# Kernel tuning notes

Hardware: AMD Instinct MI355X
Metric: run time of the kernel (lower is better)

## Reference

```python
import jax, jax.numpy as jnp
import numpy as np

BN_EPS = 1e-5

def _bn(x, p):
    # p: [4, C] = (gamma, beta, running_mean, running_var); inference-mode BN
    g, b, m, v = p[0], p[1], p[2], p[3]
    if x.ndim == 3:  # [B, C, N]
        g, b, m, v = g[:, None], b[:, None], m[:, None], v[:, None]
    return g * (x - m) * jax.lax.rsqrt(v + BN_EPS) + b

def _angle_density(xyz, npoints=32):
    # xyz: [B, N, 3]; pairwise cosine distance via a single GEMM instead of expand
    inner = jnp.einsum('bnc,bmc->bnm', xyz, xyz)            # [B, N, N]
    nrm = jnp.sqrt(jnp.sum(xyz * xyz, axis=-1))             # [B, N]
    dist = 1.0 - inner / (nrm[:, :, None] * nrm[:, None, :])
    neg_vals, _ = jax.lax.top_k(-dist, npoints)             # k smallest distances
    feat_density = jnp.mean(-neg_vals, axis=-1)             # [B, N]
    inv = 1.0 / feat_density
    return inv / jnp.max(inv)                               # global max, as in torch

def _density_attn(x, density, wqk, wt, bt, bnp):
    # x: [B, C, N]; density: [B, 1, N]; wqk: [C//4, 1] (q_conv and k_conv share weights)
    xk = wqk * density                                      # [B, C//4, N] (1x1 conv, 1 in-ch)
    energy = jnp.einsum('bdn,bdm->bnm', xk, xk)             # x_q == x_k.T (shared weight)
    attn = jax.nn.softmax(energy, axis=-1)
    attn = attn / (1e-9 + jnp.sum(attn, axis=1, keepdims=True))
    x_r = jnp.einsum('bcn,bnm->bcm', x, attn)               # [B, C, N]
    y = jnp.einsum('oc,bcn->bon', wt, x - x_r) + bt[:, None]
    return x + jax.nn.relu(_bn(y, bnp))

def _conv_bn_relu(x, w, bnp):
    return jax.nn.relu(_bn(jnp.einsum('oc,bcn->bon', w, x), bnp))

def _forward(x, w1, w2, w3, w4, w5, bn1, bn2, bn3, bn4, bn5,
             da1_wqk, da1_wt, da1_bt, da1_bn,
             da2_wqk, da2_wt, da2_bt, da2_bn,
             da3_wqk, da3_wt, da3_bt, da3_bn,
             da4_wqk, da4_wt, da4_bt, da4_bn,
             lin1_w, bn6, lin2_w, lin2_b):
    dens = _angle_density(jnp.transpose(x, (0, 2, 1)), 32)[:, None, :]  # [B, 1, N]
    h = _conv_bn_relu(x, w1, bn1)
    h = _density_attn(h, dens, da1_wqk, da1_wt, da1_bt, da1_bn)
    h = _conv_bn_relu(h, w2, bn2)
    h = _density_attn(h, dens, da2_wqk, da2_wt, da2_bt, da2_bn)
    h = _conv_bn_relu(h, w3, bn3)
    h = _density_attn(h, dens, da3_wqk, da3_wt, da3_bt, da3_bn)
    h = _conv_bn_relu(h, w4, bn4)
    h = _density_attn(h, dens, da4_wqk, da4_wt, da4_bt, da4_bn)
    h = _conv_bn_relu(h, w5, bn5)                           # [B, 1024, N]
    h = jnp.max(h, axis=-1)                                 # adaptive_max_pool1d -> [B, 1024]
    h = jax.nn.relu(_bn(h @ lin1_w.T, bn6))                 # [B, 512]; dropout is identity in eval
    return h @ lin2_w.T + lin2_b                            # [B, num_classes]

def setup_inputs() -> dict:
    key = jax.random.key(0)
    ki = iter(jax.random.split(key, 80))
    def rn(shape, s):
        return jax.random.normal(next(ki), shape, jnp.float32) * s
    def bnp(c):
        return jnp.stack([
            jax.random.uniform(next(ki), (c,), jnp.float32, 0.5, 1.5),  # gamma
            rn((c,), 0.05),                                             # beta
            rn((c,), 0.1),                                              # running_mean
            jax.random.uniform(next(ki), (c,), jnp.float32, 0.5, 1.5),  # running_var
        ])
    B, N, E = 16, 2048, 1024
    d = {}
    d['x'] = jax.random.normal(next(ki), (B, 3, N), jnp.float32)
    d['w1'] = rn((64, 3), 0.5)
    d['w2'] = rn((64, 64), 0.125)
    d['w3'] = rn((64, 64), 0.125)
    d['w4'] = rn((128, 64), 0.125)
    d['w5'] = rn((E, 128), 0.09)
    d['bn1'], d['bn2'], d['bn3'] = bnp(64), bnp(64), bnp(64)
    d['bn4'], d['bn5'] = bnp(128), bnp(E)
    for i, c in zip((1, 2, 3, 4), (64, 64, 64, 128)):
        d[f'da{i}_wqk'] = rn((c // 4, 1), 1.0)
        d[f'da{i}_wt'] = rn((c, c), 1.0 / np.sqrt(c))
        d[f'da{i}_bt'] = rn((c,), 0.05)
        d[f'da{i}_bn'] = bnp(c)
    d['lin1_w'] = rn((512, E), 1.0 / np.sqrt(E))
    d['bn6'] = bnp(512)
    d['lin2_w'] = rn((40, 512), 1.0 / np.sqrt(512))
    d['lin2_b'] = rn((40,), 0.05)
    return d

def reference(x, w1, w2, w3, w4, w5, bn1, bn2, bn3, bn4, bn5,
              da1_wqk, da1_wt, da1_bt, da1_bn,
              da2_wqk, da2_wt, da2_bt, da2_bn,
              da3_wqk, da3_wt, da3_bt, da3_bn,
              da4_wqk, da4_wt, da4_bt, da4_bn,
              lin1_w, bn6, lin2_w, lin2_b):
    return _forward(x, w1, w2, w3, w4, w5, bn1, bn2, bn3, bn4, bn5,
                    da1_wqk, da1_wt, da1_bt, da1_bn,
                    da2_wqk, da2_wt, da2_bt, da2_bn,
                    da3_wqk, da3_wt, da3_bt, da3_bn,
                    da4_wqk, da4_wt, da4_bt, da4_bn,
                    lin1_w, bn6, lin2_w, lin2_b)
```

## Files before the change

kernel.cpp:

```cpp
#include <hip/hip_runtime.h>
#include <math.h>

#define BB 16
#define NN 2048
#define BN_EPS_ 1e-5f

typedef __attribute__((ext_vector_type(8))) short short8v;
typedef __attribute__((ext_vector_type(4))) float f32x4;

__device__ __forceinline__ unsigned short f2bf(float x){
  unsigned u = __float_as_uint(x);
  u += 0x7fffu + ((u >> 16) & 1u);
  return (unsigned short)(u >> 16);
}
__device__ __forceinline__ float bf2f(unsigned short h){
  return __uint_as_float(((unsigned)h) << 16);
}

__global__ __launch_bounds__(256) void normalize_points_kernel(const float* __restrict__ x,
        float* __restrict__ u){
  int idx = blockIdx.x*256 + threadIdx.x;
  int b = idx >> 11, n = idx & (NN-1);
  const float* xb = x + (size_t)b*3*NN;
  float x0 = xb[n], x1 = xb[NN+n], x2 = xb[2*NN+n];
  float rn = rsqrtf(x0*x0 + x1*x1 + x2*x2);
  float* ub = u + (size_t)b*3*NN;
  ub[n] = x0*rn; ub[NN+n] = x1*rn; ub[2*NN+n] = x2*rn;
}

#define DG 8
__global__ __launch_bounds__(256) void density5_kernel(const float* __restrict__ u,
        float* __restrict__ inv, float* __restrict__ blockmax){
  __shared__ float us0[NN], us1[NN], us2[NN];
  __shared__ unsigned int hist[DG][256];
  __shared__ float buf[DG][128];
  __shared__ unsigned int bufcnt[DG];
  __shared__ unsigned int bB[DG], bC0[DG];
  __shared__ float partial[DG][4];
  __shared__ float rowiv[DG];
  const int b = blockIdx.y;
  const float* ub = u + (size_t)b*3*NN;
  const int t = threadIdx.x;
  #pragma unroll
  for (int i = 0; i < NN/(256*4); ++i){
    int n4 = t + 256*i;
    ((float4*)us0)[n4] = ((const float4*)ub)[n4];
    ((float4*)us1)[n4] = ((const float4*)(ub+NN))[n4];
    ((float4*)us2)[n4] = ((const float4*)(ub+2*NN))[n4];
  }
  #pragma unroll
  for (int i = 0; i < DG; ++i) hist[i][t & 255] = 0u;
  if (t < DG) bufcnt[t] = 0u;
  __syncthreads();
  float m0[8], m1[8], m2[8];
  #pragma unroll
  for (int i = 0; i < 8; ++i){
    int c = t + 256*i;
    m0[i] = us0[c]; m1[i] = us1[c]; m2[i] = us2[c];
  }
  const int r0 = blockIdx.x * DG;
  float ru0[DG], ru1[DG], ru2[DG];
  #pragma unroll
  for (int j = 0; j < DG; ++j){ ru0[j] = us0[r0+j]; ru1[j] = us1[r0+j]; ru2[j] = us2[r0+j]; }

  unsigned qp[DG][2];
  #pragma unroll
  for (int j = 0; j < DG; ++j){
    unsigned q0 = 0u, q1 = 0u;
    #pragma unroll
    for (int i = 0; i < 8; ++i){
      float d = 1.0f - (ru0[j]*m0[i] + ru1[j]*m1[i] + ru2[j]*m2[i]);
      int q = (int)(d * 128.0f);
      q = q < 0 ? 0 : (q > 255 ? 255 : q);
      if (i < 4) q0 |= (unsigned)q << (8*i); else q1 |= (unsigned)q << (8*(i-4));
      atomicAdd(&hist[j][q], 1u);
    }
    qp[j][0] = q0; qp[j][1] = q1;
  }
  __syncthreads();

  const int wave = t >> 6, lane = t & 63;
  #pragma unroll
  for (int jj = 0; jj < 2; ++jj){
    const int j = 2*wave + jj;
    uint4 cc = *(const uint4*)&hist[j][lane*4];
    unsigned tl = cc.x + cc.y + cc.z + cc.w;
    unsigned inc = tl;
    #pragma unroll
    for (int off = 1; off < 64; off <<= 1){
      unsigned o = __shfl_up(inc, off);
      if (lane >= off) inc += o;
    }
    unsigned base = inc - tl;
    if (base < 32u && base + tl >= 32u){
      unsigned cum = base;
      if (cum < 32u && cum + cc.x >= 32u){ bB[j] = lane*4 + 0; bC0[j] = cum; } cum += cc.x;
      if (cum < 32u && cum + cc.y >= 32u){ bB[j] = lane*4 + 1; bC0[j] = cum; } cum += cc.y;
      if (cum < 32u && cum + cc.z >= 32u){ bB[j] = lane*4 + 2; bC0[j] = cum; } cum += cc.z;
      if (cum < 32u && cum + cc.w >= 32u){ bB[j] = lane*4 + 3; bC0[j] = cum; } cum += cc.w;
    }
  }
  __syncthreads();

  #pragma unroll
  for (int j = 0; j < DG; ++j){
    const int B = (int)bB[j];
    float s = 0.0f;
    #pragma unroll
    for (int i = 0; i < 8; ++i){
      float d = 1.0f - (ru0[j]*m0[i] + ru1[j]*m1[i] + ru2[j]*m2[i]);
      const int q = (int)((qp[j][i>>2] >> (8*(i&3))) & 255u);
      if (q < B) s += d;
      else if (q == B){
        unsigned slot = atomicAdd(&bufcnt[j], 1u);
        if (slot < 128u) buf[j][slot] = d;
      }
    }
    #pragma unroll
    for (int off = 32; off > 0; off >>= 1) s += __shfl_xor(s, off);
    if (lane == 0) partial[j][wave] = s;
  }
  __syncthreads();

  #pragma unroll
  for (int jj = 0; jj < 2; ++jj){
    const int j = 2*wave + jj;
    float total = partial[j][0] + partial[j][1] + partial[j][2] + partial[j][3];
    int cnt = (int)bufcnt[j]; if (cnt > 128) cnt = 128;
    const int rr = 32 - (int)bC0[j];
    float v1 = (lane      < cnt) ? buf[j][lane]      : 0.0f;
    float v2 = (lane + 64 < cnt) ? buf[j][lane + 64] : 0.0f;
    int rk1 = 0, rk2 = 0;
    for (int k = 0; k < cnt; ++k){
      float vk = buf[j][k];
      rk1 += ((vk < v1) || (vk == v1 && k < lane)) ? 1 : 0;
      rk2 += ((vk < v2) || (vk == v2 && k < lane + 64)) ? 1 : 0;
    }
    float contrib = ((lane      < cnt) && (rk1 < rr)) ? v1 : 0.0f;
    contrib      += ((lane + 64 < cnt) && (rk2 < rr)) ? v2 : 0.0f;
    #pragma unroll
    for (int off = 32; off > 0; off >>= 1) contrib += __shfl_xor(contrib, off);
    total += contrib;
    if (lane == 0){
      float iv = 32.0f / total;
      inv[b*NN + r0 + j] = iv;
      rowiv[j] = iv;
    }
  }
  __syncthreads();
  if (t == 0){
    float m = rowiv[0];
    #pragma unroll
    for (int j = 1; j < DG; ++j) m = fmaxf(m, rowiv[j]);
    blockmax[blockIdx.y * gridDim.x + blockIdx.x] = m;
  }
}

__global__ __launch_bounds__(256) void finalize_max_kernel(const float* __restrict__ blockmax,
        float* __restrict__ maxout){
  __shared__ float pw[4];
  const int t = threadIdx.x;
  float m = 0.0f;
  #pragma unroll
  for (int i = 0; i < 16; ++i) m = fmaxf(m, blockmax[t + 256*i]);
  #pragma unroll
  for (int off = 32; off > 0; off >>= 1) m = fmaxf(m, __shfl_xor(m, off));
  if ((t & 63) == 0) pw[t >> 6] = m;
  __syncthreads();
  if (t == 0) *maxout = fmaxf(fmaxf(pw[0], pw[1]), fmaxf(pw[2], pw[3]));
}

__global__ void normalize_kernel(float* __restrict__ dens, const float* __restrict__ maxval){
  int i = blockIdx.x*256 + threadIdx.x;
  float mx = *maxval;
  dens[i] = dens[i] / mx;
}

__global__ __launch_bounds__(256) void zrow_kernel(const float* __restrict__ dens,
      const float* __restrict__ wqk, int K, float* __restrict__ out){
  __shared__ float ds[NN];
  const int b = blockIdx.y, t = threadIdx.x;
  float s = 0.0f;
  for (int k = 0; k < K; ++k){ float w = wqk[k]; s += w*w; }
  #pragma unroll
  for (int i = 0; i < NN/256; ++i) ds[t + 256*i] = dens[b*NN + t + 256*i];
  __syncthreads();
  const int wave = t >> 6, lane = t & 63;
  const int RPB = NN / gridDim.x;
  const int r0 = blockIdx.x * RPB;
  for (int r = r0 + wave; r < r0 + RPB; r += 4){
    float a = s * ds[r];
    float sum = 0.0f;
    #pragma unroll
    for (int i = 0; i < NN/64; ++i){
      int m = lane + 64*i;
      sum += __expf(a * ds[m]);
    }
    #pragma unroll
    for (int off = 32; off > 0; off >>= 1) sum += __shfl_xor(sum, off);
    if (lane == 0) out[b*NN + r] = 1.0f/sum;
  }
}

template<int C>
__global__ __launch_bounds__(256, 2) void attn_mfma_kernel(const unsigned short* __restrict__ Ah,
      const unsigned short* __restrict__ Al, const float* __restrict__ dens,
      const float* __restrict__ zinv, const float* __restrict__ wqk, int K,
      float* __restrict__ raw){
  constexpr int RA = C + 16;
  constexpr int RH = C / 32;
  __shared__ __align__(16) unsigned short ah[C][64], al[C][64];
  __shared__ __align__(16) unsigned short eh[64][64], el[64][64];
  const int id = blockIdx.x;
  const int b  = (id & 7) + ((id >> 8) << 3);
  const int m0 = ((id >> 3) & 31) * 64;
  const int t = threadIdx.x;
  float s = 0.0f;
  for (int k = 0; k < K; ++k){ float w = wqk[k]; s += w*w; }
  const float* db = dens + b*NN;
  const float* zb = zinv + b*NN;
  const unsigned short* Abh = Ah + (size_t)b*C*NN;
  const unsigned short* Abl = Al + (size_t)b*C*NN;
  const int ej = t >> 2, ekq = (t & 3) * 16;
  const float dmj = db[m0 + ej];
  const unsigned swe = (unsigned)((ej & 7) << 4);
  const int l = t & 63, w = t >> 6;
  const int rw = w & 1, cw = w >> 1;
  const int fc = l & 15, g = l >> 4;
  const unsigned swr = (unsigned)((fc & 7) << 4);
  short8v ones8, zero8;
  #pragma unroll
  for (int q = 0; q < 8; ++q){ ones8[q] = (short)0x3F80; zero8[q] = 0; }
  f32x4 acc[RH][2], cs[2];
  #pragma unroll
  for (int i = 0; i < RH; ++i){ acc[i][0] = (f32x4){0.f,0.f,0.f,0.f}; acc[i][1] = (f32x4){0.f,0.f,0.f,0.f}; }
  cs[0] = (f32x4){0.f,0.f,0.f,0.f}; cs[1] = (f32x4){0.f,0.f,0.f,0.f};

  for (int n0 = 0; n0 < NN; n0 += 64){
    __syncthreads();
    #pragma unroll
    for (int i = 0; i < C*8/256; ++i){
      int idx = t + 256*i;
      int row = idx >> 3, c8 = (idx & 7) * 8;
      unsigned off = (unsigned)(row*128) + (((unsigned)(c8*2)) ^ ((unsigned)((row&7)<<4)));
      *(uint4*)((char*)ah + off) = *(const uint4*)(Abh + (size_t)row*NN + n0 + c8);
      *(uint4*)((char*)al + off) = *(const uint4*)(Abl + (size_t)row*NN + n0 + c8);
    }
    {
      unsigned hp[8], lp[8];
      #pragma unroll
      for (int u = 0; u < 4; ++u){
        float4 dn = *(const float4*)(db + n0 + ekq + u*4);
        float4 zv = *(const float4*)(zb + n0 + ekq + u*4);
        float e0 = zv.x*__expf(s*dn.x*dmj), e1 = zv.y*__expf(s*dn.y*dmj);
        float e2 = zv.z*__expf(s*dn.z*dmj), e3 = zv.w*__expf(s*dn.w*dmj);
        unsigned short a0=f2bf(e0), a1=f2bf(e1), a2=f2bf(e2), a3=f2bf(e3);
        hp[u*2+0] = (unsigned)a0 | ((unsigned)a1<<16);
        hp[u*2+1] = (unsigned)a2 | ((unsigned)a3<<16);
        lp[u*2+0] = (unsigned)f2bf(e0-bf2f(a0)) | ((unsigned)f2bf(e1-bf2f(a1))<<16);
        lp[u*2+1] = (unsigned)f2bf(e2-bf2f(a2)) | ((unsigned)f2bf(e3-bf2f(a3))<<16);
      }
      unsigned row = (unsigned)(ej*128);
      unsigned o1 = row + (((unsigned)(ekq*2))      ^ swe);
      unsigned o2 = row + (((unsigned)(ekq*2 + 16)) ^ swe);
      *(uint4*)((char*)eh + o1) = make_uint4(hp[0],hp[1],hp[2],hp[3]);
      *(uint4*)((char*)eh + o2) = make_uint4(hp[4],hp[5],hp[6],hp[7]);
      *(uint4*)((char*)el + o1) = make_uint4(lp[0],lp[1],lp[2],lp[3]);
      *(uint4*)((char*)el + o2) = make_uint4(lp[4],lp[5],lp[6],lp[7]);
    }
    __syncthreads();
    #pragma unroll
    for (int kk = 0; kk < 2; ++kk){
      unsigned ko = ((unsigned)((kk*32 + g*8)*2)) ^ swr;
      short8v bh[2], bl[2], ai[RH], au[RH];
      #pragma unroll
      for (int ct = 0; ct < 2; ++ct){
        unsigned eoff = (unsigned)(((2*cw + ct)*16 + fc)*128) + ko;
        bh[ct] = *(const short8v*)((const char*)eh + eoff);
        bl[ct] = *(const short8v*)((const char*)el + eoff);
      }
      #pragma unroll
      for (int i = 0; i < RH; ++i){
        unsigned aoff = (unsigned)((rw*(C/2) + i*16 + fc)*128) + ko;
        ai[i] = *(const short8v*)((const char*)ah + aoff);
        au[i] = *(const short8v*)((const char*)al + aoff);
      }
      #pragma unroll
      for (int i = 0; i < RH; ++i){
        #pragma unroll
        for (int ct = 0; ct < 2; ++ct){
          acc[i][ct] = __builtin_amdgcn_mfma_f32_16x16x32_bf16(ai[i], bh[ct], acc[i][ct], 0, 0, 0);
          acc[i][ct] = __builtin_amdgcn_mfma_f32_16x16x32_bf16(ai[i], bl[ct], acc[i][ct], 0, 0, 0);
          acc[i][ct] = __builtin_amdgcn_mfma_f32_16x16x32_bf16(au[i], bh[ct], acc[i][ct], 0, 0, 0);
        }
      }
      if (rw == 1){
        short8v ac = (fc == 0) ? ones8 : zero8;
        #pragma unroll
        for (int ct = 0; ct < 2; ++ct){
          cs[ct] = __builtin_amdgcn_mfma_f32_16x16x32_bf16(ac, bh[ct], cs[ct], 0, 0, 0);
          cs[ct] = __builtin_amdgcn_mfma_f32_16x16x32_bf16(ac, bl[ct], cs[ct], 0, 0, 0);
        }
      }
    }
  }
  #pragma unroll
  for (int ct = 0; ct < 2; ++ct){
    float* rb = raw + (size_t)b*RA*NN + m0 + (2*cw + ct)*16 + fc;
    #pragma unroll
    for (int i = 0; i < RH; ++i){
      #pragma unroll
      for (int r = 0; r < 4; ++r){
        int row = rw*(C/2) + i*16 + g*4 + r;
        rb[(size_t)row*NN] = acc[i][ct][r];
      }
    }
    if (rw == 1){
      #pragma unroll
      for (int r = 0; r < 4; ++r){
        int row = C + g*4 + r;
        rb[(size_t)row*NN] = cs[ct][r];
      }
    }
  }
}

template<int C, bool TP>
__global__ __launch_bounds__(256) void attn_post_kernel(const float* __restrict__ x,
      const float* __restrict__ raw, const float* __restrict__ wt,
      const float* __restrict__ bt, const float* __restrict__ bnp,
      float* __restrict__ out, unsigned short* __restrict__ th,
      unsigned short* __restrict__ tl){
  constexpr int RA = C + 16;
  __shared__ float ds[32][68];
  __shared__ float ws[32][C+4];
  __shared__ float cbs[64];
  const int b = blockIdx.y, m0 = blockIdx.x*64, t = threadIdx.x;
  const float* xb = x + (size_t)b*C*NN;
  const float* rb = raw + (size_t)b*RA*NN;
  if (t < 64) cbs[t] = 1.0f / (1e-9f + rb[(size_t)C*NN + m0 + t]);
  const int tr = t >> 4, tc = t & 15;
  constexpr int R = C/16;
  float acc[R][4];
  #pragma unroll
  for (int i = 0; i < R; ++i){ acc[i][0]=acc[i][1]=acc[i][2]=acc[i][3]=0.0f; }
  for (int c0 = 0; c0 < C; c0 += 32){
    __syncthreads();
    #pragma unroll
    for (int i = 0; i < 8; ++i){
      int idx = t + 256*i;
      int m = idx & 63, cl = idx >> 6;
      int cc = c0 + cl;
      ds[cl][m] = xb[cc*NN + m0 + m] - rb[cc*NN + m0 + m] * cbs[m];
    }
    #pragma unroll
    for (int i = 0; i < C*32/256; ++i){
      int idx = t + 256*i;
      int cl = idx & 31, o = idx >> 5;
      ws[cl][o] = wt[o*C + c0 + cl];
    }
    __syncthreads();
    #pragma unroll
    for (int k = 0; k < 32; ++k){
      float4 e = *(const float4*)&ds[k][tc*4];
      float a[R];
      #pragma unroll
      for (int q = 0; q < R/4; ++q)
        *(float4*)&a[q*4] = *(const float4*)&ws[k][tr*R + q*4];
      #pragma unroll
      for (int i = 0; i < R; ++i){
        acc[i][0] += a[i]*e.x; acc[i][1] += a[i]*e.y;
        acc[i][2] += a[i]*e.z; acc[i][3] += a[i]*e.w;
      }
    }
  }
  #pragma unroll
  for (int i = 0; i < R; ++i){
    int o = tr*R + i;
    float g = bnp[o], be = bnp[C+o], mn = bnp[2*C+o], vv = bnp[3*C+o];
    float sc = g * rsqrtf(vv + BN_EPS_);
    float sh = be - mn*sc;
    float bv = bt[o];
    #pragma unroll
    for (int j = 0; j < 4; ++j){
      float y = acc[i][j] + bv;
      y = sc*y + sh;
      y = fmaxf(y, 0.0f);
      acc[i][j] = xb[o*NN + m0 + tc*4 + j] + y;
    }
    if (!TP)
      *(float4*)&out[((size_t)b*C + o)*NN + m0 + tc*4] =
          make_float4(acc[i][0], acc[i][1], acc[i][2], acc[i][3]);
  }
  if (TP){
    unsigned short* Ts = (unsigned short*)&ws[0][0];
    #pragma unroll
    for (int pass = 0; pass < 2; ++pass){
      __syncthreads();
      #pragma unroll
      for (int q = 0; q < R/2; ++q){
        #pragma unroll
        for (int j = 0; j < 4; ++j){
          int n = tc*4 + j;
          float y0 = acc[2*q][j], y1 = acc[2*q+1][j];
          unsigned short a0 = f2bf(y0), a1 = f2bf(y1);
          unsigned short v0 = pass ? f2bf(y0 - bf2f(a0)) : a0;
          unsigned short v1 = pass ? f2bf(y1 - bf2f(a1)) : a1;
          unsigned off = (unsigned)(n*256) +
              (((unsigned)((tr*R + 2*q)*2)) ^ ((unsigned)((n&7)<<4)));
          *(unsigned*)((char*)Ts + off) = (unsigned)v0 | ((unsigned)v1<<16);
        }
      }
      __syncthreads();
      unsigned short* gout = (pass ? tl : th) + ((size_t)b*NN + m0)*128;
      int n = t >> 2;
      #pragma unroll
      for (int s2 = 0; s2 < 4; ++s2){
        int sl = (t&3)*4 + s2;
        unsigned off = (unsigned)(n*256) + ((unsigned)((sl ^ (n&7)) << 4));
        uint4 v = *(const uint4*)((const char*)Ts + off);
        *(uint4*)(gout + (size_t)n*128 + sl*8) = v;
      }
    }
  }
}

template<int CIN, int COUT>
__global__ __launch_bounds__(256) void conv_bn_relu_kernel(const float* __restrict__ x,
      const float* __restrict__ w, const float* __restrict__ bnp, float* __restrict__ out,
      unsigned short* __restrict__ oh, unsigned short* __restrict__ ol){
  constexpr int CH = (CIN < 32) ? CIN : 32;
  __shared__ float xs[CH][68];
  __shared__ float ws[CH][COUT+4];
  const int b = blockIdx.y, m0 = blockIdx.x*64, t = threadIdx.x;
  const float* xb = x + (size_t)b*CIN*NN;
  const int tr = t >> 4, tc = t & 15;
  constexpr int R = COUT/16;
  float acc[R][4];
  #pragma unroll
  for (int i = 0; i < R; ++i){ acc[i][0]=acc[i][1]=acc[i][2]=acc[i][3]=0.0f; }
  for (int c0 = 0; c0 < CIN; c0 += CH){
    __syncthreads();
    for (int idx = t; idx < CH*64; idx += 256){
      int m = idx & 63, cl = idx >> 6;
      xs[cl][m] = xb[(c0+cl)*NN + m0 + m];
    }
    for (int idx = t; idx < CH*COUT; idx += 256){
      int cl = idx % CH, o = idx / CH;
      ws[cl][o] = w[o*CIN + c0 + cl];
    }
    __syncthreads();
    #pragma unroll
    for (int k = 0; k < CH; ++k){
      float4 e = *(const float4*)&xs[k][tc*4];
      float a[R];
      #pragma unroll
      for (int q = 0; q < R/4; ++q)
        *(float4*)&a[q*4] = *(const float4*)&ws[k][tr*R + q*4];
      #pragma unroll
      for (int i = 0; i < R; ++i){
        acc[i][0] += a[i]*e.x; acc[i][1] += a[i]*e.y;
        acc[i][2] += a[i]*e.z; acc[i][3] += a[i]*e.w;
      }
    }
  }
  #pragma unroll
  for (int i = 0; i < R; ++i){
    int o = tr*R + i;
    float g = bnp[o], be = bnp[COUT+o], mn = bnp[2*COUT+o], vv = bnp[3*COUT+o];
    float sc = g * rsqrtf(vv + BN_EPS_);
    float sh = be - mn*sc;
    float4 r;
    float* rp = &r.x;
    #pragma unroll
    for (int j = 0; j < 4; ++j){
      float y = sc*acc[i][j] + sh;
      rp[j] = fmaxf(y, 0.0f);
    }
    size_t base = ((size_t)b*COUT + o)*NN + m0 + tc*4;
    *(float4*)&out[base] = r;
    unsigned short h0=f2bf(r.x), h1=f2bf(r.y), h2=f2bf(r.z), h3=f2bf(r.w);
    uint2 hp, lp;
    hp.x = (unsigned)h0 | ((unsigned)h1<<16);
    hp.y = (unsigned)h2 | ((unsigned)h3<<16);
    lp.x = (unsigned)f2bf(r.x-bf2f(h0)) | ((unsigned)f2bf(r.y-bf2f(h1))<<16);
    lp.y = (unsigned)f2bf(r.z-bf2f(h2)) | ((unsigned)f2bf(r.w-bf2f(h3))<<16);
    *(uint2*)&oh[base] = hp;
    *(uint2*)&ol[base] = lp;
  }
}

__global__ __launch_bounds__(256, 2) void conv5_mfma_kernel(
      const unsigned short* __restrict__ hTh, const unsigned short* __restrict__ hTl,
      const float* __restrict__ w5, const float* __restrict__ bnp,
      float* __restrict__ pooled){
  __shared__ __align__(16) unsigned short wh[64][128], wl[64][128];
  __shared__ __align__(16) unsigned short hh[64][128], hl[64][128];
  const int id = blockIdx.x;
  const int b  = (id & 7) + ((id >> 9) << 3);
  const int inner = (id >> 3) & 63;
  const int o0 = (inner & 15) * 64;
  const int nb = (inner >> 4) * (NN/4);
  const int t = threadIdx.x;
  const int l = t & 63, w = t >> 6;
  const int rw = w & 1, cw = w >> 1;
  const int fc = l & 15, g = l >> 4;
  const unsigned swr = (unsigned)((fc & 7) << 4);
  #pragma unroll
  for (int i = 0; i < 8; ++i){
    int idx = t + 256*i;
    int row = idx >> 5, c0 = (idx & 31) * 4;
    float4 v = *(const float4*)(w5 + (size_t)(o0 + row)*128 + c0);
    unsigned short h0=f2bf(v.x), h1=f2bf(v.y), h2=f2bf(v.z), h3=f2bf(v.w);
    uint2 hp, lp;
    hp.x = (unsigned)h0 | ((unsigned)h1<<16);
    hp.y = (unsigned)h2 | ((unsigned)h3<<16);
    lp.x = (unsigned)f2bf(v.x-bf2f(h0)) | ((unsigned)f2bf(v.y-bf2f(h1))<<16);
    lp.y = (unsigned)f2bf(v.z-bf2f(h2)) | ((unsigned)f2bf(v.w-bf2f(h3))<<16);
    unsigned off = (unsigned)(row*256) + (((unsigned)(c0*2)) ^ ((unsigned)((row&7)<<4)));
    *(uint2*)((char*)wh + off) = hp;
    *(uint2*)((char*)wl + off) = lp;
  }
  float sc[2][4], sh[2][4];
  #pragma unroll
  for (int i = 0; i < 2; ++i){
    #pragma unroll
    for (int r = 0; r < 4; ++r){
      int o = o0 + rw*32 + i*16 + g*4 + r;
      float gg = bnp[o], be = bnp[1024+o], mn = bnp[2048+o], vv = bnp[3072+o];
      sc[i][r] = gg * rsqrtf(vv + BN_EPS_);
      sh[i][r] = be - mn*sc[i][r];
    }
  }
  float vmax[2][4] = {{0.f,0.f,0.f,0.f},{0.f,0.f,0.f,0.f}};
  const unsigned short* hb = hTh + (size_t)b*NN*128;
  const unsigned short* lb = hTl + (size_t)b*NN*128;
  for (int nt = 0; nt < (NN/4)/64; ++nt){
    const int n0 = nb + nt*64;
    __syncthreads();
    #pragma unroll
    for (int i = 0; i < 4; ++i){
      int idx = t + 256*i;
      int row = idx >> 4, sl = idx & 15;
      unsigned off = (unsigned)(row*256) + ((unsigned)((sl << 4) ^ ((row&7)<<4)));
      *(uint4*)((char*)hh + off) = *(const uint4*)(hb + (size_t)(n0+row)*128 + sl*8);
      *(uint4*)((char*)hl + off) = *(const uint4*)(lb + (size_t)(n0+row)*128 + sl*8);
    }
    __syncthreads();
    f32x4 acc[2][2];
    #pragma unroll
    for (int i = 0; i < 2; ++i){ acc[i][0] = (f32x4){0.f,0.f,0.f,0.f}; acc[i][1] = (f32x4){0.f,0.f,0.f,0.f}; }
    #pragma unroll
    for (int kk = 0; kk < 4; ++kk){
      unsigned ko = ((unsigned)((kk*32 + g*8)*2)) ^ swr;
      short8v aih[2], ail[2], bih[2], bil[2];
      #pragma unroll
      for (int i = 0; i < 2; ++i){
        unsigned aoff = (unsigned)((rw*32 + i*16 + fc)*256) + ko;
        aih[i] = *(const short8v*)((const char*)wh + aoff);
        ail[i] = *(const short8v*)((const char*)wl + aoff);
      }
      #pragma unroll
      for (int ct = 0; ct < 2; ++ct){
        unsigned boff = (unsigned)((cw*32 + ct*16 + fc)*256) + ko;
        bih[ct] = *(const short8v*)((const char*)hh + boff);
        bil[ct] = *(const short8v*)((const char*)hl + boff);
      }
      #pragma unroll
      for (int i = 0; i < 2; ++i){
        #pragma unroll
        for (int ct = 0; ct < 2; ++ct){
          acc[i][ct] = __builtin_amdgcn_mfma_f32_16x16x32_bf16(aih[i], bih[ct], acc[i][ct], 0, 0, 0);
          acc[i][ct] = __builtin_amdgcn_mfma_f32_16x16x32_bf16(aih[i], bil[ct], acc[i][ct], 0, 0, 0);
          acc[i][ct] = __builtin_amdgcn_mfma_f32_16x16x32_bf16(ail[i], bih[ct], acc[i][ct], 0, 0, 0);
        }
      }
    }
    #pragma unroll
    for (int i = 0; i < 2; ++i){
      #pragma unroll
      for (int ct = 0; ct < 2; ++ct){
        #pragma unroll
        for (int r = 0; r < 4; ++r){
          float y = sc[i][r]*acc[i][ct][r] + sh[i][r];
          y = fmaxf(y, 0.0f);
          vmax[i][r] = fmaxf(vmax[i][r], y);
        }
      }
    }
  }
  #pragma unroll
  for (int i = 0; i < 2; ++i){
    #pragma unroll
    for (int r = 0; r < 4; ++r){
      float v = vmax[i][r];
      v = fmaxf(v, __shfl_xor(v, 1));
      v = fmaxf(v, __shfl_xor(v, 2));
      v = fmaxf(v, __shfl_xor(v, 4));
      v = fmaxf(v, __shfl_xor(v, 8));
      if (fc == 0)
        atomicMax((unsigned int*)&pooled[b*1024 + o0 + rw*32 + i*16 + g*4 + r],
                  __float_as_uint(v));
    }
  }
}

__global__ void lin1_kernel(const float* __restrict__ pooled, const float* __restrict__ w,
      const float* __restrict__ bnp, float* __restrict__ out1){
  int tid = blockIdx.x*256 + threadIdx.x;
  int b = tid >> 9, j = tid & 511;
  const float4* p4 = (const float4*)(pooled + b*1024);
  const float4* w4 = (const float4*)(w + j*1024);
  float sum = 0.0f;
  for (int e = 0; e < 256; ++e){
    float4 a = p4[e], c = w4[e];
    sum += a.x*c.x + a.y*c.y + a.z*c.z + a.w*c.w;
  }
  float g = bnp[j], be = bnp[512+j], mn = bnp[2*512+j], vv = bnp[3*512+j];
  float s = g * rsqrtf(vv + BN_EPS_);
  float y = s*sum + (be - mn*s);
  out1[b*512 + j] = fmaxf(y, 0.0f);
}

__global__ void lin2_kernel(const float* __restrict__ h, const float* __restrict__ w,
      const float* __restrict__ bias, float* __restrict__ out){
  int tid = blockIdx.x*64 + threadIdx.x;
  if (tid >= 640) return;
  int b = tid / 40, k = tid % 40;
  const float4* h4 = (const float4*)(h + b*512);
  const float4* w4 = (const float4*)(w + k*512);
  float sum = 0.0f;
  for (int e = 0; e < 128; ++e){
    float4 a = h4[e], c = w4[e];
    sum += a.x*c.x + a.y*c.y + a.z*c.z + a.w*c.w;
  }
  out[tid] = sum + bias[k];
}

extern "C" void kernel_launch(void* const* d_in, const int* in_sizes, int n_in,
                              void* d_out, int out_size, void* d_ws, size_t ws_size,
                              hipStream_t stream){
  (void)in_sizes; (void)n_in; (void)out_size; (void)ws_size;
  const float* x     = (const float*)d_in[0];
  const float* w1    = (const float*)d_in[1];
  const float* w2    = (const float*)d_in[2];
  const float* w3    = (const float*)d_in[3];
  const float* w4    = (const float*)d_in[4];
  const float* w5    = (const float*)d_in[5];
  const float* bn1   = (const float*)d_in[6];
  const float* bn2   = (const float*)d_in[7];
  const float* bn3   = (const float*)d_in[8];
  const float* bn4   = (const float*)d_in[9];
  const float* bn5   = (const float*)d_in[10];
  const float* da_wqk[4] = {(const float*)d_in[11], (const float*)d_in[15], (const float*)d_in[19], (const float*)d_in[23]};
  const float* da_wt[4]  = {(const float*)d_in[12], (const float*)d_in[16], (const float*)d_in[20], (const float*)d_in[24]};
  const float* da_bt[4]  = {(const float*)d_in[13], (const float*)d_in[17], (const float*)d_in[21], (const float*)d_in[25]};
  const float* da_bn[4]  = {(const float*)d_in[14], (const float*)d_in[18], (const float*)d_in[22], (const float*)d_in[26]};
  const float* lin1_w = (const float*)d_in[27];
  const float* bn6    = (const float*)d_in[28];
  const float* lin2_w = (const float*)d_in[29];
  const float* lin2_b = (const float*)d_in[30];

  float* ws = (float*)d_ws;
  float* maxval = ws;
  float* dens   = ws + 64;
  float* zinv   = dens + BB*NN;
  float* hA     = zinv + BB*NN;
  float* hB     = hA  + (size_t)BB*64*NN;
  float* h4A    = hB  + (size_t)BB*64*NN;
  float* raw    = h4A + (size_t)BB*128*NN;
  float* pooled = raw + (size_t)BB*144*NN;
  float* l1o    = pooled + BB*1024;
  float* uvec   = l1o + BB*512;
  float* blockmax = uvec + (size_t)BB*3*NN;
  unsigned short* Ah = (unsigned short*)(blockmax + 4096);
  unsigned short* Al = Ah + (size_t)BB*128*NN;
  float* h4B    = hA;

  normalize_points_kernel<<<dim3(BB*NN/256), 256, 0, stream>>>(x, uvec);
  density5_kernel<<<dim3(NN/DG, BB), 256, 0, stream>>>(uvec, dens, blockmax);
  finalize_max_kernel<<<dim3(1), 256, 0, stream>>>(blockmax, maxval);
  normalize_kernel<<<dim3(BB*NN/256), 256, 0, stream>>>(dens, maxval);

  conv_bn_relu_kernel<3,64><<<dim3(32,BB),256,0,stream>>>(x, w1, bn1, hA, Ah, Al);

  zrow_kernel<<<dim3(32,BB),256,0,stream>>>(dens, da_wqk[0], 16, zinv);
  attn_mfma_kernel<64><<<dim3(512),256,0,stream>>>(Ah, Al, dens, zinv, da_wqk[0], 16, raw);
  attn_post_kernel<64,false><<<dim3(32,BB),256,0,stream>>>(hA, raw, da_wt[0], da_bt[0], da_bn[0], hB, nullptr, nullptr);

  conv_bn_relu_kernel<64,64><<<dim3(32,BB),256,0,stream>>>(hB, w2, bn2, hA, Ah, Al);

  zrow_kernel<<<dim3(32,BB),256,0,stream>>>(dens, da_wqk[1], 16, zinv);
  attn_mfma_kernel<64><<<dim3(512),256,0,stream>>>(Ah, Al, dens, zinv, da_wqk[1], 16, raw);
  attn_post_kernel<64,false><<<dim3(32,BB),256,0,stream>>>(hA, raw, da_wt[1], da_bt[1], da_bn[1], hB, nullptr, nullptr);

  conv_bn_relu_kernel<64,64><<<dim3(32,BB),256,0,stream>>>(hB, w3, bn3, hA, Ah, Al);

  zrow_kernel<<<dim3(32,BB),256,0,stream>>>(dens, da_wqk[2], 16, zinv);
  attn_mfma_kernel<64><<<dim3(512),256,0,stream>>>(Ah, Al, dens, zinv, da_wqk[2], 16, raw);
  attn_post_kernel<64,false><<<dim3(32,BB),256,0,stream>>>(hA, raw, da_wt[2], da_bt[2], da_bn[2], hB, nullptr, nullptr);

  conv_bn_relu_kernel<64,128><<<dim3(32,BB),256,0,stream>>>(hB, w4, bn4, h4A, Ah, Al);

  zrow_kernel<<<dim3(32,BB),256,0,stream>>>(dens, da_wqk[3], 32, zinv);
  attn_mfma_kernel<128><<<dim3(512),256,0,stream>>>(Ah, Al, dens, zinv, da_wqk[3], 32, raw);
  attn_post_kernel<128,true><<<dim3(32,BB),256,0,stream>>>(h4A, raw, da_wt[3], da_bt[3], da_bn[3], h4B, Ah, Al);

  hipMemsetAsync(pooled, 0, BB*1024*sizeof(float), stream);
  conv5_mfma_kernel<<<dim3(1024),256,0,stream>>>(Ah, Al, w5, bn5, pooled);
  lin1_kernel<<<dim3(32),256,0,stream>>>(pooled, lin1_w, bn6, l1o);
  lin2_kernel<<<dim3(10),64,0,stream>>>(l1o, lin2_w, lin2_b, (float*)d_out);
}
```

Measured before the change: 596.7 us.

## Compute attention weights in registers and prefetch next A tile

Drops the shared-memory staging of the exp-weight tile. Each lane now computes its own B-operand fragment directly in registers, at the cost of redundant exp work across the row-waves. It also software-pipelines the global loads of the next A tile into registers while the current tile's MFMAs run. It adds s_setprio around the MFMA blocks. The intent is to cut LDS traffic and barriers and to hide global-load latency, while raising register pressure and duplicated transcendental work.

```diff
diff --git a/kernel.cpp b/kernel.cpp
--- a/kernel.cpp
+++ b/kernel.cpp
@@ -209,8 +209,8 @@
       float* __restrict__ raw){
   constexpr int RA = C + 16;
   constexpr int RH = C / 32;
+  constexpr int NL = C*8/256;
   __shared__ __align__(16) unsigned short ah[C][64], al[C][64];
-  __shared__ __align__(16) unsigned short eh[64][64], el[64][64];
   const int id = blockIdx.x;
   const int b  = (id & 7) + ((id >> 8) << 3);
   const int m0 = ((id >> 3) & 31) * 64;
@@ -221,13 +221,13 @@
   const float* zb = zinv + b*NN;
   const unsigned short* Abh = Ah + (size_t)b*C*NN;
   const unsigned short* Abl = Al + (size_t)b*C*NN;
-  const int ej = t >> 2, ekq = (t & 3) * 16;
-  const float dmj = db[m0 + ej];
-  const unsigned swe = (unsigned)((ej & 7) << 4);
   const int l = t & 63, w = t >> 6;
   const int rw = w & 1, cw = w >> 1;
   const int fc = l & 15, g = l >> 4;
   const unsigned swr = (unsigned)((fc & 7) << 4);
+  float dm[2];
+  dm[0] = s * db[m0 + (2*cw+0)*16 + fc];
+  dm[1] = s * db[m0 + (2*cw+1)*16 + fc];
   short8v ones8, zero8;
   #pragma unroll
   for (int q = 0; q < 8; ++q){ ones8[q] = (short)0x3F80; zero8[q] = 0; }
@@ -236,49 +236,39 @@
   for (int i = 0; i < RH; ++i){ acc[i][0] = (f32x4){0.f,0.f,0.f,0.f}; acc[i][1] = (f32x4){0.f,0.f,0.f,0.f}; }
   cs[0] = (f32x4){0.f,0.f,0.f,0.f}; cs[1] = (f32x4){0.f,0.f,0.f,0.f};
 
-  for (int n0 = 0; n0 < NN; n0 += 64){
+  uint4 pah[NL], pal[NL];
+  auto loadA = [&](int n0){
+    #pragma unroll
+    for (int i = 0; i < NL; ++i){
+      int idx = t + 256*i;
+      int row = idx >> 3, c8 = (idx & 7) * 8;
+      pah[i] = *(const uint4*)(Abh + (size_t)row*NN + n0 + c8);
+      pal[i] = *(const uint4*)(Abl + (size_t)row*NN + n0 + c8);
+    }
+  };
+  loadA(0);
+  for (int tix = 0; tix < NN/64; ++tix){
+    const int n0 = tix * 64;
     __syncthreads();
     #pragma unroll
-    for (int i = 0; i < C*8/256; ++i){
+    for (int i = 0; i < NL; ++i){
       int idx = t + 256*i;
       int row = idx >> 3, c8 = (idx & 7) * 8;
       unsigned off = (unsigned)(row*128) + (((unsigned)(c8*2)) ^ ((unsigned)((row&7)<<4)));
-      *(uint4*)((char*)ah + off) = *(const uint4*)(Abh + (size_t)row*NN + n0 + c8);
-      *(uint4*)((char*)al + off) = *(const uint4*)(Abl + (size_t)row*NN + n0 + c8);
-    }
-    {
-      unsigned hp[8], lp[8];
-      #pragma unroll
-      for (int u = 0; u < 4; ++u){
-        float4 dn = *(const float4*)(db + n0 + ekq + u*4);
-        float4 zv = *(const float4*)(zb + n0 + ekq + u*4);
-        float e0 = zv.x*__expf(s*dn.x*dmj), e1 = zv.y*__expf(s*dn.y*dmj);
-        float e2 = zv.z*__expf(s*dn.z*dmj), e3 = zv.w*__expf(s*dn.w*dmj);
-        unsigned short a0=f2bf(e0), a1=f2bf(e1), a2=f2bf(e2), a3=f2bf(e3);
-        hp[u*2+0] = (unsigned)a0 | ((unsigned)a1<<16);
-        hp[u*2+1] = (unsigned)a2 | ((unsigned)a3<<16);
-        lp[u*2+0] = (unsigned)f2bf(e0-bf2f(a0)) | ((unsigned)f2bf(e1-bf2f(a1))<<16);
-        lp[u*2+1] = (unsigned)f2bf(e2-bf2f(a2)) | ((unsigned)f2bf(e3-bf2f(a3))<<16);
-      }
-      unsigned row = (unsigned)(ej*128);
-      unsigned o1 = row + (((unsigned)(ekq*2))      ^ swe);
-      unsigned o2 = row + (((unsigned)(ekq*2 + 16)) ^ swe);
-      *(uint4*)((char*)eh + o1) = make_uint4(hp[0],hp[1],hp[2],hp[3]);
-      *(uint4*)((char*)eh + o2) = make_uint4(hp[4],hp[5],hp[6],hp[7]);
-      *(uint4*)((char*)el + o1) = make_uint4(lp[0],lp[1],lp[2],lp[3]);
-      *(uint4*)((char*)el + o2) = make_uint4(lp[4],lp[5],lp[6],lp[7]);
+      *(uint4*)((char*)ah + off) = pah[i];
+      *(uint4*)((char*)al + off) = pal[i];
     }
     __syncthreads();
+    if (tix + 1 < NN/64) loadA(n0 + 64);
     #pragma unroll
     for (int kk = 0; kk < 2; ++kk){
+      const int kb = n0 + kk*32 + g*8;
+      float4 dn0 = *(const float4*)(db + kb);
+      float4 dn1 = *(const float4*)(db + kb + 4);
+      float4 zv0 = *(const float4*)(zb + kb);
+      float4 zv1 = *(const float4*)(zb + kb + 4);
       unsigned ko = ((unsigned)((kk*32 + g*8)*2)) ^ swr;
-      short8v bh[2], bl[2], ai[RH], au[RH];
-      #pragma unroll
-      for (int ct = 0; ct < 2; ++ct){
-        unsigned eoff = (unsigned)(((2*cw + ct)*16 + fc)*128) + ko;
-        bh[ct] = *(const short8v*)((const char*)eh + eoff);
-        bl[ct] = *(const short8v*)((const char*)el + eoff);
-      }
+      short8v ai[RH], au[RH];
       #pragma unroll
       for (int i = 0; i < RH; ++i){
         unsigned aoff = (unsigned)((rw*(C/2) + i*16 + fc)*128) + ko;
@@ -286,21 +276,32 @@
         au[i] = *(const short8v*)((const char*)al + aoff);
       }
       #pragma unroll
-      for (int i = 0; i < RH; ++i){
+      for (int ct = 0; ct < 2; ++ct){
+        float e[8];
+        e[0] = zv0.x*__expf(dn0.x*dm[ct]); e[1] = zv0.y*__expf(dn0.y*dm[ct]);
+        e[2] = zv0.z*__expf(dn0.z*dm[ct]); e[3] = zv0.w*__expf(dn0.w*dm[ct]);
+        e[4] = zv1.x*__expf(dn1.x*dm[ct]); e[5] = zv1.y*__expf(dn1.y*dm[ct]);
+        e[6] = zv1.z*__expf(dn1.z*dm[ct]); e[7] = zv1.w*__expf(dn1.w*dm[ct]);
+        short8v bh, bl;
         #pragma unroll
-        for (int ct = 0; ct < 2; ++ct){
-          acc[i][ct] = __builtin_amdgcn_mfma_f32_16x16x32_bf16(ai[i], bh[ct], acc[i][ct], 0, 0, 0);
-          acc[i][ct] = __builtin_amdgcn_mfma_f32_16x16x32_bf16(ai[i], bl[ct], acc[i][ct], 0, 0, 0);
-          acc[i][ct] = __builtin_amdgcn_mfma_f32_16x16x32_bf16(au[i], bh[ct], acc[i][ct], 0, 0, 0);
+        for (int j = 0; j < 8; ++j){
+          unsigned short hj = f2bf(e[j]);
+          bh[j] = (short)hj;
+          bl[j] = (short)f2bf(e[j] - bf2f(hj));
         }
-      }
-      if (rw == 1){
-        short8v ac = (fc == 0) ? ones8 : zero8;
+        __builtin_amdgcn_s_setprio(1);
         #pragma unroll
-        for (int ct = 0; ct < 2; ++ct){
-          cs[ct] = __builtin_amdgcn_mfma_f32_16x16x32_bf16(ac, bh[ct], cs[ct], 0, 0, 0);
-          cs[ct] = __builtin_amdgcn_mfma_f32_16x16x32_bf16(ac, bl[ct], cs[ct], 0, 0, 0);
+        for (int i = 0; i < RH; ++i){
+          acc[i][ct] = __builtin_amdgcn_mfma_f32_16x16x32_bf16(ai[i], bh, acc[i][ct], 0, 0, 0);
+          acc[i][ct] = __builtin_amdgcn_mfma_f32_16x16x32_bf16(ai[i], bl, acc[i][ct], 0, 0, 0);
+          acc[i][ct] = __builtin_amdgcn_mfma_f32_16x16x32_bf16(au[i], bh, acc[i][ct], 0, 0, 0);
         }
+        if (rw == 1){
+          short8v ac = (fc == 0) ? ones8 : zero8;
+          cs[ct] = __builtin_amdgcn_mfma_f32_16x16x32_bf16(ac, bh, cs[ct], 0, 0, 0);
+          cs[ct] = __builtin_amdgcn_mfma_f32_16x16x32_bf16(ac, bl, cs[ct], 0, 0, 0);
+        }
+        __builtin_amdgcn_s_setprio(0);
       }
     }
   }
```

Result: slower. 820.4 us (+37.5%).
